# Performance work log

Measured on AMD Instinct MI355X. Metric: run time of the kernel, lower is better.

The kernel has to match this reference:

```python
import jax, jax.numpy as jnp
import numpy as np
import math

EMBED = 1024
HEADS = 16
HEAD_DIM = EMBED // HEADS


def setup_inputs() -> dict:
    key = jax.random.key(0)
    ks = jax.random.split(key, 9)
    B, S = 2, 2048
    query = jax.random.normal(ks[0], (B, S, EMBED), dtype=jnp.float32)
    key_t = jax.random.normal(ks[1], (B, S, EMBED), dtype=jnp.float32)
    value = jax.random.normal(ks[2], (B, S, EMBED), dtype=jnp.float32)
    mask = jax.random.randint(ks[3], (B, 1, S, S), 0, 2, dtype=jnp.int32)
    # nn.Linear(head_dim, head_dim, bias=False) weights: [out, in]
    sc = 1.0 / math.sqrt(HEAD_DIM)
    Wq = jax.random.uniform(ks[4], (HEAD_DIM, HEAD_DIM), jnp.float32, -sc, sc)
    Wk = jax.random.uniform(ks[5], (HEAD_DIM, HEAD_DIM), jnp.float32, -sc, sc)
    Wv = jax.random.uniform(ks[6], (HEAD_DIM, HEAD_DIM), jnp.float32, -sc, sc)
    so = 1.0 / math.sqrt(EMBED)
    Wo = jax.random.uniform(ks[7], (EMBED, EMBED), jnp.float32, -so, so)
    bo = jax.random.uniform(ks[8], (EMBED,), jnp.float32, -so, so)
    return {"query": query, "key": key_t, "value": value, "mask": mask,
            "Wq": Wq, "Wk": Wk, "Wv": Wv, "Wo": Wo, "bo": bo}


def reference(query, key, value, mask, Wq, Wk, Wv, Wo, bo):
    B, Sq, E = query.shape
    Sk = key.shape[1]
    H, D = HEADS, HEAD_DIM
    # Faithful raw reshape into heads (as in the torch source, no transpose)
    q = query.reshape(B, H, Sq, D)
    k = key.reshape(B, H, Sk, D)
    v = value.reshape(B, H, Sk, D)
    # per-head_dim Linear (bias-free): x @ W.T
    Q = jnp.einsum('bhsd,ed->bhse', q, Wq)
    K = jnp.einsum('bhsd,ed->bhse', k, Wk)
    V = jnp.einsum('bhsd,ed->bhse', v, Wv)
    scores = jnp.einsum('bhqd,bhkd->bhqk', Q, K)  # [B,H,Sq,Sk]
    scores = jnp.where(mask == 0, jnp.float32(-1e20), scores)
    # NOTE: source divides by sqrt(embed_size), not sqrt(head_dim)
    attn = jax.nn.softmax(scores / jnp.float32(math.sqrt(E)), axis=-1)
    out = jnp.einsum('bhqk,bhkd->bhqd', attn, V).reshape(B, Sq, H * D)
    return out @ Wo.T + bo
```

## Files before the change

### kernel.cpp

```cpp
#include <hip/hip_runtime.h>

typedef __attribute__((ext_vector_type(8))) short short8;
typedef __attribute__((ext_vector_type(4))) float f32x4;
typedef __attribute__((ext_vector_type(2))) int int2v;
typedef __attribute__((ext_vector_type(4))) int int4v;

__device__ __forceinline__ short f2bf(float f) {
  unsigned u = __builtin_bit_cast(unsigned, f);
  u += 0x7fff + ((u >> 16) & 1);
  return (short)(u >> 16);
}

__device__ __forceinline__ int pk2bf(float lo, float hi) {
#if defined(__gfx950__) && __has_builtin(__builtin_amdgcn_cvt_pk_bf16_f32)
  typedef __attribute__((ext_vector_type(2))) __bf16 bf16x2;
  bf16x2 v = __builtin_amdgcn_cvt_pk_bf16_f32(lo, hi);
  return __builtin_bit_cast(int, v);
#else
  return (int)(unsigned short)(short)f2bf(lo) | (((int)f2bf(hi)) << 16);
#endif
}

__device__ __forceinline__ short8 pack8(f32x4 a, f32x4 b) {
  int4v t;
  t.x = pk2bf(a[0], a[1]);
  t.y = pk2bf(a[2], a[3]);
  t.z = pk2bf(b[0], b[1]);
  t.w = pk2bf(b[2], b[3]);
  return __builtin_bit_cast(short8, t);
}

__device__ __forceinline__ float fand(float p, int m) {
  return __builtin_bit_cast(float, __builtin_bit_cast(int, p) & m);
}

__device__ __forceinline__ int bmask(unsigned nib, int bit) {
#if __has_builtin(__builtin_amdgcn_sbfe)
  return __builtin_amdgcn_sbfe((int)nib, bit, 1);
#else
  return -(int)((nib >> bit) & 1);
#endif
}

__device__ __forceinline__ float fexp2(float x) {
#if __has_builtin(__builtin_amdgcn_exp2f)
  return __builtin_amdgcn_exp2f(x);
#else
  return exp2f(x);
#endif
}

__device__ __forceinline__ void glds16(const short* g, short* lbase, int lane) {
#if __has_builtin(__builtin_amdgcn_global_load_lds)
  __builtin_amdgcn_global_load_lds(
      (const __attribute__((address_space(1))) unsigned int*)g,
      (__attribute__((address_space(3))) unsigned int*)lbase, 16, 0, 0);
#else
  *(short8*)(lbase + lane * 8) = *(const short8*)g;
#endif
}

__global__ __launch_bounds__(256) void prep(const float* __restrict__ q,
                                            const float* __restrict__ k,
                                            const float* __restrict__ v,
                                            const float* __restrict__ Wq,
                                            const float* __restrict__ Wk,
                                            const float* __restrict__ Wv,
                                            const float* __restrict__ Wo,
                                            const int* __restrict__ mask,
                                            short* __restrict__ Qp,
                                            short* __restrict__ Kp,
                                            short* __restrict__ Vtp,
                                            short* __restrict__ Wob,
                                            unsigned long long* __restrict__ mpk) {
  const int bid = blockIdx.x;
  const int tid = threadIdx.x;

  if (bid >= 4096) {
#pragma unroll
    for (int it = 0; it < 4; ++it) {
      const int gid = ((bid - 4096) * 4 + it) * 256 + tid;
      const int base = gid & ~63, j = gid & 63;
      const int val = mask[base + ((j & 3) << 4) + (j >> 2)];
      const unsigned long long bal = __ballot(val != 0);
      if (j == 0) mpk[gid >> 6] = bal;
    }
    return;
  }
  if (bid >= 3072) {
    const int i = ((bid - 3072) * 256 + tid) * 4;
    const f32x4 x = *(const f32x4*)&Wo[i];
    int2v o;
    o.x = pk2bf(x[0], x[1]);
    o.y = pk2bf(x[2], x[3]);
    *(int2v*)&Wob[i] = o;
    return;
  }

  __shared__ short xt[64][72];
  __shared__ short ot[64][72];
  const int mode = bid >> 10;
  const int bt = bid & 1023;
  const float* X;
  const float* W;
  float scale;
  if (mode == 0) { X = q; W = Wq; scale = 0.045084220f; }
  else if (mode == 1) { X = k; W = Wk; scale = 1.0f; }
  else { X = v; W = Wv; scale = 1.0f; }

  const int r0 = bt * 64;
  const int row = tid >> 2, seg = (tid & 3) * 16;
  const f32x4* xs = (const f32x4*)(X + (r0 + row) * 64 + seg);
  const f32x4 x0 = xs[0], x1 = xs[1], x2 = xs[2], x3 = xs[3];
  *(short8*)&xt[row][seg] = pack8(x0, x1);
  *(short8*)&xt[row][seg + 8] = pack8(x2, x3);
  __syncthreads();

  const int lane = tid & 63, wave = tid >> 6;
  const int m16 = lane & 15, quad = lane >> 4;

  const short8 a0 = *(const short8*)&xt[wave * 16 + m16][quad * 8];
  const short8 a1 = *(const short8*)&xt[wave * 16 + m16][32 + quad * 8];

  f32x4 acc[4];
#pragma unroll
  for (int nt = 0; nt < 4; ++nt) {
    const f32x4* wp0 = (const f32x4*)&W[(nt * 16 + m16) * 64 + quad * 8];
    const f32x4* wp1 = (const f32x4*)&W[(nt * 16 + m16) * 64 + 32 + quad * 8];
    const short8 b0 = pack8(wp0[0], wp0[1]);
    const short8 b1 = pack8(wp1[0], wp1[1]);
    f32x4 z = (f32x4){0.f, 0.f, 0.f, 0.f};
    z = __builtin_amdgcn_mfma_f32_16x16x32_bf16(a0, b0, z, 0, 0, 0);
    z = __builtin_amdgcn_mfma_f32_16x16x32_bf16(a1, b1, z, 0, 0, 0);
    acc[nt] = z;
  }

  if (mode != 2) {
#pragma unroll
    for (int nt = 0; nt < 4; ++nt)
#pragma unroll
      for (int r = 0; r < 4; ++r)
        ot[wave * 16 + quad * 4 + r][nt * 16 + m16] = f2bf(acc[nt][r] * scale);
  } else {
#pragma unroll
    for (int nt = 0; nt < 4; ++nt)
#pragma unroll
      for (int r = 0; r < 4; ++r)
        ot[nt * 16 + m16][16 * quad + 4 * r + wave] = f2bf(acc[nt][r]);
  }
  __syncthreads();

  const int orow = tid >> 2, opart = tid & 3;
  if (mode != 2) {
    short* dst = (mode == 0 ? Qp : Kp) + (r0 + orow) * 64 + opart * 16;
    *(short8*)&dst[0] = *(const short8*)&ot[orow][opart * 16];
    *(short8*)&dst[8] = *(const short8*)&ot[orow][opart * 16 + 8];
  } else {
    const int bh = r0 >> 11, s0 = r0 & 2047;
    short* dst = Vtp + bh * 131072 + orow * 2048 + s0 + opart * 16;
    *(short8*)&dst[0] = *(const short8*)&ot[orow][opart * 16];
    *(short8*)&dst[8] = *(const short8*)&ot[orow][opart * 16 + 8];
  }
}

__global__ __launch_bounds__(256) void flashp(const short* __restrict__ Qp,
                                              const short* __restrict__ Kp,
                                              const short* __restrict__ Vt,
                                              const unsigned long long* __restrict__ mpk,
                                              short* __restrict__ O) {
  __shared__ __attribute__((aligned(16))) short kt[2][4096];
  __shared__ __attribute__((aligned(16))) short vt[2][4096];
  __shared__ __attribute__((aligned(16))) short pt[128][72];
  const int tid = threadIdx.x;
  const int bid = blockIdx.x;
  const int local = bid >> 3;
  const int bh = (bid & 7) * 4 + (local >> 4);
  const int q0 = (local & 15) << 7;
  const int b = bh >> 4;
  const short* Qh = Qp + bh * 131072;
  const short* Kh = Kp + bh * 131072;
  const short* Vh = Vt + bh * 131072;
  const int lane = tid & 63, wave = tid >> 6;
  const int m16 = lane & 15, quad = lane >> 4;
  const int srow = lane >> 3, sj = (lane & 7) ^ srow;
  const int msh = m16 * 4;
  const int koff = m16 * 128 + ((quad ^ (m16 & 7)) * 16);

  short8 aq[2][2];
#pragma unroll
  for (int g = 0; g < 2; ++g)
#pragma unroll
    for (int h = 0; h < 2; ++h)
      aq[g][h] = *(const short8*)&Qh[(q0 + wave * 32 + g * 16 + m16) * 64 + h * 32 + quad * 8];

  const unsigned long long* mq = mpk + (b * 2048 + q0 + wave * 32 + quad * 4) * 32;

  float l[2][4];
  f32x4 oacc[2][4];
#pragma unroll
  for (int g = 0; g < 2; ++g)
#pragma unroll
    for (int r = 0; r < 4; ++r) l[g][r] = 0.f;
#pragma unroll
  for (int g = 0; g < 2; ++g)
#pragma unroll
    for (int dt = 0; dt < 4; ++dt) oacc[g][dt] = (f32x4){0.f, 0.f, 0.f, 0.f};

  auto stage = [&](int buf, int ka) {
#pragma unroll
    for (int t = 0; t < 2; ++t) {
      const int crow = wave * 16 + t * 8;
      glds16(Kh + (ka * 64 + crow + srow) * 64 + sj * 8, &kt[buf][crow * 64], lane);
      glds16(Vh + (crow + srow) * 2048 + ka * 64 + sj * 8, &vt[buf][crow * 64], lane);
    }
  };
  auto lmask = [&](unsigned long long (&mw)[2][4], int ka) {
#pragma unroll
    for (int g = 0; g < 2; ++g)
#pragma unroll
      for (int r = 0; r < 4; ++r) mw[g][r] = mq[g * 512 + r * 32 + ka];
  };

  auto body = [&](int ka, int buf, unsigned long long (&mwU)[2][4],
                  unsigned long long (&mwN)[2][4]) {
    __syncthreads();
    if (ka < 31) {
      stage(buf ^ 1, ka + 1);
      lmask(mwN, ka + 1);
    }

    f32x4 s[2][4];
#pragma unroll
    for (int nt = 0; nt < 4; ++nt) {
      const int o0 = nt * 2048 + koff;
      const short8 kb0 = *(const short8*)((const char*)&kt[buf][0] + o0);
      const short8 kb1 = *(const short8*)((const char*)&kt[buf][0] + (o0 ^ 64));
#pragma unroll
      for (int g = 0; g < 2; ++g) {
        f32x4 z = (f32x4){0.f, 0.f, 0.f, 0.f};
        z = __builtin_amdgcn_mfma_f32_16x16x32_bf16(aq[g][0], kb0, z, 0, 0, 0);
        z = __builtin_amdgcn_mfma_f32_16x16x32_bf16(aq[g][1], kb1, z, 0, 0, 0);
        s[g][nt] = z;
      }
    }

#pragma unroll
    for (int g = 0; g < 2; ++g) {
#pragma unroll
      for (int r = 0; r < 4; ++r) {
        const unsigned nib = (unsigned)(mwU[g][r] >> msh) & 15u;
        const float p0 = fand(fexp2(s[g][0][r]), bmask(nib, 0));
        const float p1 = fand(fexp2(s[g][1][r]), bmask(nib, 1));
        const float p2 = fand(fexp2(s[g][2][r]), bmask(nib, 2));
        const float p3 = fand(fexp2(s[g][3][r]), bmask(nib, 3));
        l[g][r] += (p0 + p1) + (p2 + p3);
        int2v pp;
        pp.x = pk2bf(p0, p1);
        pp.y = pk2bf(p2, p3);
        *(int2v*)&pt[wave * 32 + g * 16 + quad * 4 + r][msh] = pp;
      }
    }

    short8 ap[2][2];
#pragma unroll
    for (int g = 0; g < 2; ++g)
#pragma unroll
      for (int h = 0; h < 2; ++h)
        ap[g][h] = *(const short8*)&pt[wave * 32 + g * 16 + m16][h * 32 + quad * 8];

#pragma unroll
    for (int dt = 0; dt < 4; ++dt) {
      const int o0 = dt * 2048 + koff;
      const short8 vb0 = *(const short8*)((const char*)&vt[buf][0] + o0);
      const short8 vb1 = *(const short8*)((const char*)&vt[buf][0] + (o0 ^ 64));
#pragma unroll
      for (int g = 0; g < 2; ++g) {
        f32x4 z = oacc[g][dt];
        z = __builtin_amdgcn_mfma_f32_16x16x32_bf16(ap[g][0], vb0, z, 0, 0, 0);
        z = __builtin_amdgcn_mfma_f32_16x16x32_bf16(ap[g][1], vb1, z, 0, 0, 0);
        oacc[g][dt] = z;
      }
    }
  };

  unsigned long long mwA[2][4], mwB[2][4];
  stage(0, 0);
  lmask(mwA, 0);

  for (int kk = 0; kk < 16; ++kk) {
    body(2 * kk, 0, mwA, mwB);
    body(2 * kk + 1, 1, mwB, mwA);
  }

#pragma unroll
  for (int g = 0; g < 2; ++g)
#pragma unroll
    for (int r = 0; r < 4; ++r) {
#pragma unroll
      for (int off = 1; off < 16; off <<= 1) l[g][r] += __shfl_xor(l[g][r], off, 16);
      const float inv = 1.0f / l[g][r];
#pragma unroll
      for (int dt = 0; dt < 4; ++dt)
        pt[wave * 32 + g * 16 + quad * 4 + r][dt * 16 + m16] = f2bf(oacc[g][dt][r] * inv);
    }

  const int orow = lane >> 1, opart = lane & 1;
  const int prow = wave * 32 + orow;
  short* og = O + (bh * 2048 + q0 + prow) * 64 + opart * 32;
#pragma unroll
  for (int c = 0; c < 32; c += 8)
    *(short8*)&og[c] = *(const short8*)&pt[prow][opart * 32 + c];
}

__global__ __launch_bounds__(256) void outproj(const short* __restrict__ Ob,
                                               const short* __restrict__ Wob,
                                               const float* __restrict__ bo,
                                               float* __restrict__ out) {
  __shared__ short at[64][72];
  __shared__ short bt[128][72];
  const int tid = threadIdx.x;
  const int bid = blockIdx.x;
  const int ct = bid >> 6, rt = bid & 63;
  const int r0 = rt * 64, c0 = ct * 128;
  const int lane = tid & 63, wave = tid >> 6;
  const int mr = (wave >> 1) * 32, nc = (wave & 1) * 64;
  const int m16 = lane & 15, quad = lane >> 4;
  const int arow = tid >> 2, apart = tid & 3;
  const int brow = tid >> 1, bhalf = (tid & 1) * 32;

  f32x4 acc[2][4];
#pragma unroll
  for (int mt = 0; mt < 2; ++mt)
#pragma unroll
    for (int nt = 0; nt < 4; ++nt) acc[mt][nt] = (f32x4){0.f, 0.f, 0.f, 0.f};

  for (int kc = 0; kc < 16; ++kc) {
    __syncthreads();
    const short* ag = &Ob[(r0 + arow) * 1024 + kc * 64 + apart * 16];
    const short* bg = &Wob[(c0 + brow) * 1024 + kc * 64 + bhalf];
    *(short8*)&at[arow][apart * 16] = *(const short8*)&ag[0];
    *(short8*)&at[arow][apart * 16 + 8] = *(const short8*)&ag[8];
    *(short8*)&bt[brow][bhalf] = *(const short8*)&bg[0];
    *(short8*)&bt[brow][bhalf + 8] = *(const short8*)&bg[8];
    *(short8*)&bt[brow][bhalf + 16] = *(const short8*)&bg[16];
    *(short8*)&bt[brow][bhalf + 24] = *(const short8*)&bg[24];
    __syncthreads();

#pragma unroll
    for (int kh = 0; kh < 2; ++kh) {
      short8 af[2], bf[4];
#pragma unroll
      for (int i = 0; i < 2; ++i)
        af[i] = *(const short8*)&at[mr + i * 16 + m16][kh * 32 + quad * 8];
#pragma unroll
      for (int j = 0; j < 4; ++j)
        bf[j] = *(const short8*)&bt[nc + j * 16 + m16][kh * 32 + quad * 8];
#pragma unroll
      for (int mt = 0; mt < 2; ++mt)
#pragma unroll
        for (int nt = 0; nt < 4; ++nt)
          acc[mt][nt] = __builtin_amdgcn_mfma_f32_16x16x32_bf16(af[mt], bf[nt], acc[mt][nt], 0, 0, 0);
    }
  }

#pragma unroll
  for (int nt = 0; nt < 4; ++nt) {
    const int col = c0 + nc + nt * 16 + m16;
    const float bias = bo[col];
#pragma unroll
    for (int mt = 0; mt < 2; ++mt)
#pragma unroll
      for (int rr = 0; rr < 4; ++rr)
        out[(r0 + mr + mt * 16 + quad * 4 + rr) * 1024 + col] = acc[mt][nt][rr] + bias;
  }
}

extern "C" void kernel_launch(void* const* d_in, const int* in_sizes, int n_in,
                              void* d_out, int out_size, void* d_ws, size_t ws_size,
                              hipStream_t stream) {
  const float* query = (const float*)d_in[0];
  const float* key = (const float*)d_in[1];
  const float* value = (const float*)d_in[2];
  const int* mask = (const int*)d_in[3];
  const float* Wq = (const float*)d_in[4];
  const float* Wk = (const float*)d_in[5];
  const float* Wv = (const float*)d_in[6];
  const float* Wo = (const float*)d_in[7];
  const float* bo = (const float*)d_in[8];
  float* out = (float*)d_out;

  char* ws = (char*)d_ws;
  short* Qp = (short*)(ws);
  short* Kp = (short*)(ws + 8388608);
  short* Vt = (short*)(ws + 16777216);
  short* Ob = (short*)(ws + 25165824);
  short* Wob = (short*)(ws + 33554432);
  unsigned long long* mpk = (unsigned long long*)(ws + 35651584);

  prep<<<12288, 256, 0, stream>>>(query, key, value, Wq, Wk, Wv, Wo, mask,
                                  Qp, Kp, Vt, Wob, mpk);
  flashp<<<512, 256, 0, stream>>>(Qp, Kp, Vt, mpk, Ob);
  outproj<<<512, 256, 0, stream>>>(Ob, Wob, bo, out);
}
```

Baseline: 247.8 us.

## Split attention over key halves and pre-swizzle mask bits per lane

The flash attention kernel now splits the key sequence into two halves, launching twice as many blocks. Each block writes a normalized partial output plus its row sums, and a new combine kernel merges the two halves weighted by the row sums. The mask is repacked in prep into one 32-bit word per thread per key tile, in the exact lane order the softmax consumes, which replaces the per-row 64-bit loads and shifts. The extra partial-output traffic and a fourth kernel launch are traded for more parallelism (512 blocks becomes 1024) and cheaper mask handling. Exact per-half normalization without a max subtraction relies on the scores staying bounded.

```diff
diff --git a/kernel.cpp b/kernel.cpp
--- a/kernel.cpp
+++ b/kernel.cpp
@@ -34,20 +34,16 @@
   return __builtin_bit_cast(float, __builtin_bit_cast(int, p) & m);
 }
 
-__device__ __forceinline__ int bmask(unsigned nib, int bit) {
-#if __has_builtin(__builtin_amdgcn_sbfe)
-  return __builtin_amdgcn_sbfe((int)nib, bit, 1);
-#else
-  return -(int)((nib >> bit) & 1);
-#endif
-}
-
 __device__ __forceinline__ float fexp2(float x) {
 #if __has_builtin(__builtin_amdgcn_exp2f)
   return __builtin_amdgcn_exp2f(x);
 #else
   return exp2f(x);
 #endif
+}
+
+__device__ __forceinline__ float bf2f(short s) {
+  return __builtin_bit_cast(float, ((int)(unsigned short)s) << 16);
 }
 
 __device__ __forceinline__ void glds16(const short* g, short* lbase, int lane) {
@@ -72,19 +68,25 @@
                                             short* __restrict__ Kp,
                                             short* __restrict__ Vtp,
                                             short* __restrict__ Wob,
-                                            unsigned long long* __restrict__ mpk) {
+                                            unsigned* __restrict__ mmod) {
   const int bid = blockIdx.x;
   const int tid = threadIdx.x;
 
   if (bid >= 4096) {
-#pragma unroll
-    for (int it = 0; it < 4; ++it) {
-      const int gid = ((bid - 4096) * 4 + it) * 256 + tid;
-      const int base = gid & ~63, j = gid & 63;
-      const int val = mask[base + ((j & 3) << 4) + (j >> 2)];
-      const unsigned long long bal = __ballot(val != 0);
-      if (j == 0) mpk[gid >> 6] = bal;
-    }
+    const int mb = bid - 4096;
+    const int ka = mb & 31, bq = mb >> 5;
+    const int b_ = bq >> 4, qb = bq & 15;
+    const int wv = tid >> 6, qd = (tid >> 4) & 3, m16_ = tid & 15;
+    const int* mbase = mask + b_ * 4194304 + (qb * 128 + wv * 32) * 2048 + ka * 64 + m16_;
+    unsigned d = 0;
+#pragma unroll
+    for (int p = 0; p < 8; ++p) {
+      const int* mr = mbase + ((p >> 2) * 16 + qd * 4 + (p & 3)) * 2048;
+#pragma unroll
+      for (int bb = 0; bb < 4; ++bb)
+        if (mr[bb * 16] != 0) d |= 1u << (p * 4 + bb);
+    }
+    mmod[mb * 256 + tid] = d;
     return;
   }
   if (bid >= 3072) {
@@ -163,19 +165,22 @@
   }
 }
 
-__global__ __launch_bounds__(256) void flashp(const short* __restrict__ Qp,
+__global__ __launch_bounds__(256) void flashs(const short* __restrict__ Qp,
                                               const short* __restrict__ Kp,
                                               const short* __restrict__ Vt,
-                                              const unsigned long long* __restrict__ mpk,
-                                              short* __restrict__ O) {
+                                              const unsigned* __restrict__ mmod,
+                                              short* __restrict__ Opart,
+                                              float* __restrict__ lpart) {
   __shared__ __attribute__((aligned(16))) short kt[2][4096];
   __shared__ __attribute__((aligned(16))) short vt[2][4096];
   __shared__ __attribute__((aligned(16))) short pt[128][72];
   const int tid = threadIdx.x;
   const int bid = blockIdx.x;
   const int local = bid >> 3;
-  const int bh = (bid & 7) * 4 + (local >> 4);
-  const int q0 = (local & 15) << 7;
+  const int khalf = local & 1;
+  const int qblk = (local >> 1) & 15;
+  const int bh = (bid & 7) * 4 + (local >> 5);
+  const int q0 = qblk << 7;
   const int b = bh >> 4;
   const short* Qh = Qp + bh * 131072;
   const short* Kh = Kp + bh * 131072;
@@ -185,6 +190,7 @@
   const int srow = lane >> 3, sj = (lane & 7) ^ srow;
   const int msh = m16 * 4;
   const int koff = m16 * 128 + ((quad ^ (m16 & 7)) * 16);
+  const unsigned* mqb = mmod + (b * 16 + qblk) * 32 * 256 + tid;
 
   short8 aq[2][2];
 #pragma unroll
@@ -193,8 +199,6 @@
     for (int h = 0; h < 2; ++h)
       aq[g][h] = *(const short8*)&Qh[(q0 + wave * 32 + g * 16 + m16) * 64 + h * 32 + quad * 8];
 
-  const unsigned long long* mq = mpk + (b * 2048 + q0 + wave * 32 + quad * 4) * 32;
-
   float l[2][4];
   f32x4 oacc[2][4];
 #pragma unroll
@@ -205,6 +209,8 @@
   for (int g = 0; g < 2; ++g)
 #pragma unroll
     for (int dt = 0; dt < 4; ++dt) oacc[g][dt] = (f32x4){0.f, 0.f, 0.f, 0.f};
+
+  const int kaEnd = khalf * 16 + 15;
 
   auto stage = [&](int buf, int ka) {
 #pragma unroll
@@ -214,19 +220,12 @@
       glds16(Vh + (crow + srow) * 2048 + ka * 64 + sj * 8, &vt[buf][crow * 64], lane);
     }
   };
-  auto lmask = [&](unsigned long long (&mw)[2][4], int ka) {
-#pragma unroll
-    for (int g = 0; g < 2; ++g)
-#pragma unroll
-      for (int r = 0; r < 4; ++r) mw[g][r] = mq[g * 512 + r * 32 + ka];
-  };
-
-  auto body = [&](int ka, int buf, unsigned long long (&mwU)[2][4],
-                  unsigned long long (&mwN)[2][4]) {
+
+  auto body = [&](int ka, int buf, unsigned mwU, unsigned& mwN) {
     __syncthreads();
-    if (ka < 31) {
+    if (ka < kaEnd) {
       stage(buf ^ 1, ka + 1);
-      lmask(mwN, ka + 1);
+      mwN = mqb[(ka + 1) * 256];
     }
 
     f32x4 s[2][4];
@@ -248,15 +247,17 @@
     for (int g = 0; g < 2; ++g) {
 #pragma unroll
       for (int r = 0; r < 4; ++r) {
-        const unsigned nib = (unsigned)(mwU[g][r] >> msh) & 15u;
-        const float p0 = fand(fexp2(s[g][0][r]), bmask(nib, 0));
-        const float p1 = fand(fexp2(s[g][1][r]), bmask(nib, 1));
-        const float p2 = fand(fexp2(s[g][2][r]), bmask(nib, 2));
-        const float p3 = fand(fexp2(s[g][3][r]), bmask(nib, 3));
-        l[g][r] += (p0 + p1) + (p2 + p3);
+        const int pb = (g * 4 + r) * 4;
+        float p[4];
+#pragma unroll
+        for (int nt = 0; nt < 4; ++nt) {
+          const int m = ((int)(mwU << (31 - (pb + nt)))) >> 31;
+          p[nt] = fand(fexp2(s[g][nt][r]), m);
+        }
+        l[g][r] += (p[0] + p[1]) + (p[2] + p[3]);
         int2v pp;
-        pp.x = pk2bf(p0, p1);
-        pp.y = pk2bf(p2, p3);
+        pp.x = pk2bf(p[0], p[1]);
+        pp.y = pk2bf(p[2], p[3]);
         *(int2v*)&pt[wave * 32 + g * 16 + quad * 4 + r][msh] = pp;
       }
     }
@@ -283,15 +284,18 @@
     }
   };
 
-  unsigned long long mwA[2][4], mwB[2][4];
-  stage(0, 0);
-  lmask(mwA, 0);
-
-  for (int kk = 0; kk < 16; ++kk) {
-    body(2 * kk, 0, mwA, mwB);
-    body(2 * kk + 1, 1, mwB, mwA);
-  }
-
+  unsigned mwA, mwB = 0;
+  const int ka0 = khalf * 16;
+  stage(0, ka0);
+  mwA = mqb[ka0 * 256];
+
+  for (int kk = 0; kk < 8; ++kk) {
+    body(ka0 + 2 * kk, 0, mwA, mwB);
+    body(ka0 + 2 * kk + 1, 1, mwB, mwA);
+  }
+
+  short* Oh = Opart + khalf * 4194304;
+  float* lh = lpart + khalf * 65536;
 #pragma unroll
   for (int g = 0; g < 2; ++g)
 #pragma unroll
@@ -302,14 +306,38 @@
 #pragma unroll
       for (int dt = 0; dt < 4; ++dt)
         pt[wave * 32 + g * 16 + quad * 4 + r][dt * 16 + m16] = f2bf(oacc[g][dt][r] * inv);
+      if (m16 == 0) lh[bh * 2048 + q0 + wave * 32 + g * 16 + quad * 4 + r] = l[g][r];
     }
 
   const int orow = lane >> 1, opart = lane & 1;
   const int prow = wave * 32 + orow;
-  short* og = O + (bh * 2048 + q0 + prow) * 64 + opart * 32;
+  short* og = Oh + (bh * 2048 + q0 + prow) * 64 + opart * 32;
 #pragma unroll
   for (int c = 0; c < 32; c += 8)
     *(short8*)&og[c] = *(const short8*)&pt[prow][opart * 32 + c];
+}
+
+__global__ __launch_bounds__(256) void combineO(const short* __restrict__ O0,
+                                                const short* __restrict__ O1,
+                                                const float* __restrict__ lp,
+                                                short* __restrict__ Ob) {
+  const int gid = blockIdx.x * 256 + threadIdx.x;
+  const int e0 = gid * 8;
+  const int row = e0 >> 6;
+  const float l1 = lp[row], l2 = lp[65536 + row];
+  const float is = 1.0f / (l1 + l2);
+  const float w1 = l1 * is, w2 = l2 * is;
+  const short8 a = *(const short8*)&O0[e0];
+  const short8 c = *(const short8*)&O1[e0];
+  float f[8];
+#pragma unroll
+  for (int j = 0; j < 8; ++j) f[j] = w1 * bf2f(a[j]) + w2 * bf2f(c[j]);
+  int4v o;
+  o.x = pk2bf(f[0], f[1]);
+  o.y = pk2bf(f[2], f[3]);
+  o.z = pk2bf(f[4], f[5]);
+  o.w = pk2bf(f[6], f[7]);
+  *(short8*)&Ob[e0] = __builtin_bit_cast(short8, o);
 }
 
 __global__ __launch_bounds__(256) void outproj(const short* __restrict__ Ob,
@@ -393,12 +421,15 @@
   short* Qp = (short*)(ws);
   short* Kp = (short*)(ws + 8388608);
   short* Vt = (short*)(ws + 16777216);
-  short* Ob = (short*)(ws + 25165824);
-  short* Wob = (short*)(ws + 33554432);
-  unsigned long long* mpk = (unsigned long long*)(ws + 35651584);
-
-  prep<<<12288, 256, 0, stream>>>(query, key, value, Wq, Wk, Wv, Wo, mask,
-                                  Qp, Kp, Vt, Wob, mpk);
-  flashp<<<512, 256, 0, stream>>>(Qp, Kp, Vt, mpk, Ob);
+  short* Opart = (short*)(ws + 25165824);
+  short* Wob = (short*)(ws + 41943040);
+  float* lp = (float*)(ws + 44040192);
+  unsigned* mmod = (unsigned*)(ws + 44564480);
+  short* Ob = Qp;
+
+  prep<<<5120, 256, 0, stream>>>(query, key, value, Wq, Wk, Wv, Wo, mask,
+                                 Qp, Kp, Vt, Wob, mmod);
+  flashs<<<1024, 256, 0, stream>>>(Qp, Kp, Vt, mmod, Opart, lp);
+  combineO<<<2048, 256, 0, stream>>>(Opart, Opart + 4194304, lp, Ob);
   outproj<<<512, 256, 0, stream>>>(Ob, Wob, bo, out);
 }
```

Measured after the change: 246.3 us. About the same (-0.6%).
